# Optimization experiments

Measured on AMD Instinct MI355X. Metric: run time of the kernel, lower is better.

The kernel has to match this reference:

```python
import jax, jax.numpy as jnp
import numpy as np
from jax import lax


def _conv(x, w, b):
    # x: (B,C,H,W), w: (O,I,3,3) -> SAME padding, stride 1 (NCHW/OIHW)
    y = lax.conv_general_dilated(x, w, (1, 1), 'SAME',
                                 dimension_numbers=('NCHW', 'OIHW', 'NCHW'))
    return y + b[None, :, None, None]


def _maxpool2(x):
    return lax.reduce_window(x, -jnp.inf, lax.max, (1, 1, 2, 2), (1, 1, 2, 2), 'VALID')


def setup_inputs() -> dict:
    key = jax.random.key(0)
    ks = jax.random.split(key, 16)
    B, C, H, W = 4096, 3, 32, 32
    E, NC = 4, 10
    s = 0.05
    x = jax.random.normal(ks[0], (B, C, H, W), jnp.float32)
    return {
        'x': x,
        # gating network
        'gw_conv': jax.random.normal(ks[1], (16, C, 3, 3), jnp.float32) * s,
        'gb_conv': jnp.zeros((16,), jnp.float32),
        'gw_fc': jax.random.normal(ks[2], (E, 16), jnp.float32) * s,
        'gb_fc': jnp.zeros((E,), jnp.float32),
        # experts (stacked over leading expert dim E)
        'ew_conv1': jax.random.normal(ks[3], (E, 32, C, 3, 3), jnp.float32) * s,
        'eb_conv1': jnp.zeros((E, 32), jnp.float32),
        'ew_conv2': jax.random.normal(ks[4], (E, 64, 32, 3, 3), jnp.float32) * s,
        'eb_conv2': jnp.zeros((E, 64), jnp.float32),
        'ew_fc1': jax.random.normal(ks[5], (E, 128, 64 * 8 * 8), jnp.float32) * s,
        'eb_fc1': jnp.zeros((E, 128), jnp.float32),
        'ew_fc2': jax.random.normal(ks[6], (E, NC, 128), jnp.float32) * s,
        'eb_fc2': jnp.zeros((E, NC), jnp.float32),
    }


def reference(x, gw_conv, gb_conv, gw_fc, gb_fc,
              ew_conv1, eb_conv1, ew_conv2, eb_conv2,
              ew_fc1, eb_fc1, ew_fc2, eb_fc2):
    B = x.shape[0]
    E = gw_fc.shape[0]
    NC = ew_fc2.shape[1]
    TOP_K = 1

    # ---- Router: conv -> relu -> global avg pool -> linear -> softmax ----
    h = jax.nn.relu(_conv(x, gw_conv, gb_conv))          # (B,16,32,32)
    pooled = h.mean(axis=(2, 3))                          # (B,16)
    router_probs = jax.nn.softmax(pooled @ gw_fc.T + gb_fc, axis=1)  # (B,E)

    # ---- Top-k hard routing -> dense per-expert combine weights ----
    topk_probs, topk_idx = lax.top_k(router_probs, TOP_K)  # (B,k)
    weights = jnp.zeros((B, E), x.dtype).at[
        jnp.arange(B)[:, None], topk_idx].add(topk_probs)  # (B,E), zero off-topk

    # ---- Experts: run each expert densely, weight, accumulate ----
    # (expert_out * 0 == 0 exactly, so this matches torch's gather/scatter-add)
    final = jnp.zeros((B, NC), x.dtype)
    for i in range(E):  # small fixed expert count
        h1 = _maxpool2(jax.nn.relu(_conv(x, ew_conv1[i], eb_conv1[i])))   # (B,32,16,16)
        h2 = _maxpool2(jax.nn.relu(_conv(h1, ew_conv2[i], eb_conv2[i])))  # (B,64,8,8)
        f = h2.reshape(B, -1)                                             # (B,4096)
        f = jax.nn.relu(f @ ew_fc1[i].T + eb_fc1[i])                      # (B,128)
        out = f @ ew_fc2[i].T + eb_fc2[i]                                 # (B,NC)
        final = final + out * weights[:, i:i + 1]

    # ---- Load-balancing auxiliary loss (MSE vs uniform) ----
    mean_probs = router_probs.mean(axis=0)
    aux_loss = jnp.mean((mean_probs - 1.0 / E) ** 2)
    return final, router_probs, aux_loss
```

## Files before the change

kernel.cpp:

```cpp
#include <hip/hip_runtime.h>
#include <hip/hip_bf16.h>
#include <cstdint>
#include <cstddef>

#define B_N 4096
typedef short short8 __attribute__((ext_vector_type(8)));
typedef float f32x4 __attribute__((ext_vector_type(4)));
typedef float f32x2 __attribute__((ext_vector_type(2)));

static constexpr size_t H2B_OFF    = 0;
static constexpr size_t POOLED_OFF = 8388608;
static constexpr size_t EIDX_OFF   = POOLED_OFF + (size_t)B_N * 16;
static constexpr size_t EW_OFF     = EIDX_OFF + B_N;
static constexpr size_t ORDER_OFF  = EW_OFF + B_N;
static constexpr size_t CNT_OFF    = ORDER_OFF + (size_t)4 * B_N;
static constexpr size_t PSUM_OFF   = CNT_OFF + 4;
static constexpr size_t W2R_OFF    = PSUM_OFF + 4;
static constexpr size_t W1R_OFF    = W2R_OFF + 36864;
static constexpr size_t W1C_OFF    = W1R_OFF + 1048576;

__device__ __forceinline__ unsigned int f2bf(float f) {
  unsigned int u = __float_as_uint(f);
  return (u + 0x7fffu + ((u >> 16) & 1u)) >> 16;
}
__device__ __forceinline__ unsigned int pkbf(float lo, float hi) {
  float2 f; f.x = lo; f.y = hi;
  __hip_bfloat162 b = __float22bfloat162_rn(f);
  union { __hip_bfloat162 b; unsigned u; } c; c.b = b; return c.u;
}

__global__ __launch_bounds__(256) void k_front(
    const float* __restrict__ wfc1, unsigned short* __restrict__ w1r,
    const float* __restrict__ wc2, unsigned short* __restrict__ w2r,
    const float* __restrict__ wc1, unsigned short* __restrict__ w1c,
    int* __restrict__ counts) {
  const int rb = blockIdx.x, t = threadIdx.x;
  if (rb < 2048) {
    const int i = rb * 256 + t;
    const float4 v = ((const float4*)wfc1)[i];
    ushort4 u;
    u.x = (unsigned short)f2bf(v.x); u.y = (unsigned short)f2bf(v.y);
    u.z = (unsigned short)f2bf(v.z); u.w = (unsigned short)f2bf(v.w);
    *(ushort4*)(w1r + 4 * (size_t)i) = u;
  } else if (rb < 2336) {
    if (rb == 2048 && t < 8) counts[t] = 0;
    const int i = (rb - 2048) * 256 + t;
    if (i < 4 * 9 * 64 * 32) {
      const int ic = i & 31, j = i >> 5;
      const int oc = j & 63, j2 = j >> 6;
      const int s = j2 % 9, e = j2 / 9;
      w2r[i] = (unsigned short)f2bf(wc2[(((size_t)e * 64 + oc) * 32 + ic) * 9 + s]);
    }
  } else {
    const int i = (rb - 2336) * 256 + t;
    if (i < 4096) {
      const int j = i & 7, n16 = (i >> 3) & 15, q = (i >> 7) & 3, nt = (i >> 9) & 1, e = i >> 10;
      const int k = q * 8 + j;
      float v = 0.f;
      if (k < 27) {
        const int ky = k / 9, c = k % 9, kx = c / 3, ic = c % 3;
        v = wc1[((e * 32 + nt * 16 + n16) * 3 + ic) * 9 + ky * 3 + kx];
      }
      w1c[i] = (unsigned short)f2bf(v);
    }
  }
}

__device__ __forceinline__ short8 gather_a(const float* __restrict__ base,
                                           const int* goff, bool isq1, bool isq3) {
  const float a0 = base[goff[0]];
  float       a1 = base[goff[0] + 1];
  const float b0 = base[goff[1]], b1 = base[goff[1] + 1];
  const float c0 = base[goff[2]], c1 = base[goff[2] + 1];
  const float d0 = base[goff[3]], d1 = base[goff[3] + 1];
  a1 = isq1 ? base[102] : a1;
  union { unsigned u[4]; short8 s; } r;
  r.u[0] = pkbf(a0, a1);
  r.u[1] = pkbf(b0, isq3 ? 0.f : b1);
  r.u[2] = isq3 ? 0u : pkbf(c0, c1);
  r.u[3] = isq3 ? 0u : pkbf(d0, d1);
  return r.s;
}

__global__ __launch_bounds__(256, 3) void k_experts_conv(const float* __restrict__ x,
    const float* __restrict__ gw, const float* __restrict__ gb,
    const float* __restrict__ gwfc, const float* __restrict__ gbfc,
    const unsigned short* __restrict__ w1c, const float* __restrict__ b1g,
    const unsigned short* __restrict__ w2r, const float* __restrict__ b2g,
    unsigned short* __restrict__ h2b, float* __restrict__ probs_out,
    float* __restrict__ ewt, int* __restrict__ counts, int* __restrict__ order) {
  __shared__ __align__(16) float xpi[3572];
  __shared__ __align__(16) unsigned short h1s[18 * 18 * 36];
  __shared__ float red[16 * 33];
  __shared__ float pooled_s[16];
  __shared__ int es;
  const int b = blockIdx.x, t = threadIdx.x;
  {
    uint4 z4 = make_uint4(0, 0, 0, 0);
    uint4* z1 = (uint4*)h1s;
    for (int i = t; i < 1458; i += 256) z1[i] = z4;
    uint4* z2 = (uint4*)xpi;
    for (int i = t; i < 893; i += 256) z2[i] = z4;
  }
  __syncthreads();
  const float4* x4 = (const float4*)(x + (size_t)b * 3072);
  for (int i = t; i < 768; i += 256) {
    float4 v = x4[i];
    int flat = i * 4, ic = flat >> 10, rem = flat & 1023, row = rem >> 5, col = rem & 31;
    float* d = &xpi[(row + 1) * 102 + (col + 1) * 3 + ic];
    d[0] = v.x; d[3] = v.y; d[6] = v.z; d[9] = v.w;
  }
  __syncthreads();
  {
    const int ty = t >> 4, tx = t & 15;
    f32x2 wp[3][4][3];
#pragma unroll
    for (int ic = 0; ic < 3; ++ic)
#pragma unroll
    for (int rr = 0; rr < 4; ++rr) {
      const float* p = &xpi[(2 * ty + rr) * 102 + (2 * tx) * 3 + ic];
      const float r0 = p[0], r1 = p[3], r2 = p[6], r3 = p[9];
      wp[ic][rr][0] = (f32x2){r0, r1};
      wp[ic][rr][1] = (f32x2){r1, r2};
      wp[ic][rr][2] = (f32x2){r2, r3};
    }
    float sums[16];
#pragma unroll
    for (int oc = 0; oc < 16; ++oc) {
      const float bias = gb[oc];
      f32x2 A0 = {bias, bias};
      f32x2 A1 = {bias, bias};
#pragma unroll
      for (int ic = 0; ic < 3; ++ic)
#pragma unroll
      for (int ky = 0; ky < 3; ++ky)
#pragma unroll
      for (int kx = 0; kx < 3; ++kx) {
        const float wv2 = gw[oc * 27 + ic * 9 + ky * 3 + kx];
        const f32x2 ws = {wv2, wv2};
        A0 = __builtin_elementwise_fma(wp[ic][ky][kx], ws, A0);
        A1 = __builtin_elementwise_fma(wp[ic][ky + 1][kx], ws, A1);
      }
      sums[oc] = fmaxf(A0.x, 0.f) + fmaxf(A0.y, 0.f) + fmaxf(A1.x, 0.f) + fmaxf(A1.y, 0.f);
    }
    const int rl = t & 63, wid = t >> 6;
#pragma unroll
    for (int oc = 0; oc < 16; ++oc) {
      float s = sums[oc];
      s += __shfl_xor(s, 1);
      s += __shfl_xor(s, 2);
      s += __shfl_xor(s, 4);
      sums[oc] = s;
    }
    if ((rl & 7) == 0) {
      const int slot = wid * 8 + (rl >> 3);
#pragma unroll
      for (int oc = 0; oc < 16; ++oc) red[oc * 33 + slot] = sums[oc];
    }
    __syncthreads();
    if (t < 16) {
      float s = 0.f;
#pragma unroll
      for (int i = 0; i < 32; ++i) s += red[t * 33 + i];
      pooled_s[t] = s * (1.f / 1024.f);
    }
    __syncthreads();
    if (t == 0) {
      float l[4];
#pragma unroll
      for (int j = 0; j < 4; ++j) {
        float s = gbfc[j];
#pragma unroll
        for (int i = 0; i < 16; ++i) s += pooled_s[i] * gwfc[j * 16 + i];
        l[j] = s;
      }
      const float mx = fmaxf(fmaxf(l[0], l[1]), fmaxf(l[2], l[3]));
      float ex[4], ssum = 0.f;
#pragma unroll
      for (int j = 0; j < 4; ++j) { ex[j] = expf(l[j] - mx); ssum += ex[j]; }
      const float inv = 1.f / ssum;
      float p[4];
#pragma unroll
      for (int j = 0; j < 4; ++j) p[j] = ex[j] * inv;
      *(float4*)(probs_out + (size_t)b * 4) = make_float4(p[0], p[1], p[2], p[3]);
      int em = 0; float pm = p[0];
#pragma unroll
      for (int j = 1; j < 4; ++j) if (p[j] > pm) { pm = p[j]; em = j; }
      ewt[b] = pm;
      const int slot = atomicAdd(&counts[em], 1);
      order[em * B_N + slot] = b;
      es = em;
    }
    __syncthreads();
  }
  const int e = __builtin_amdgcn_readfirstlane(es);
  const int lane = t & 63, wv = t >> 6;
  const int n16 = lane & 15, q = lane >> 4;
  {
    const bool isq1 = (q == 1), isq3 = (q == 3);
    const short8 wb0 = *(const short8*)(w1c + (((e * 2 + 0) * 4 + q) * 16 + n16) * 8);
    const short8 wb1 = *(const short8*)(w1c + (((e * 2 + 1) * 4 + q) * 16 + n16) * 8);
    const float bias0 = b1g[e * 32 + n16];
    const float bias1 = b1g[e * 32 + 16 + n16];
    int goff[4];
#pragma unroll
    for (int t4 = 0; t4 < 4; ++t4) {
      const int p0 = q * 8 + 2 * t4;
      const int r = (p0 * 939) >> 13;
      goff[t4] = r * 102 + (p0 - 9 * r);
    }
    for (int pid = 0; pid < 8; ++pid) {
      const int pairid = wv * 8 + pid;
      const int yp = pairid >> 1, xh = pairid & 1;
      const float* baseA = &xpi[(2 * yp) * 102 + (xh * 16 + n16) * 3];
      const short8 afA = gather_a(baseA, goff, isq1, isq3);
      const short8 afB = gather_a(baseA + 102, goff, isq1, isq3);
      f32x4 aA0 = {bias0, bias0, bias0, bias0}, aA1 = {bias1, bias1, bias1, bias1};
      f32x4 aB0 = aA0, aB1 = aA1;
      aA0 = __builtin_amdgcn_mfma_f32_16x16x32_bf16(afA, wb0, aA0, 0, 0, 0);
      aA1 = __builtin_amdgcn_mfma_f32_16x16x32_bf16(afA, wb1, aA1, 0, 0, 0);
      aB0 = __builtin_amdgcn_mfma_f32_16x16x32_bf16(afB, wb0, aB0, 0, 0, 0);
      aB1 = __builtin_amdgcn_mfma_f32_16x16x32_bf16(afB, wb1, aB1, 0, 0, 0);
      const int px = xh * 8 + 2 * q;
      unsigned short* hw = &h1s[((yp + 1) * 18 + (px + 1)) * 36];
      const float p00 = fmaxf(fmaxf(fmaxf(aA0[0], aA0[1]), fmaxf(aB0[0], aB0[1])), 0.f);
      const float p01 = fmaxf(fmaxf(fmaxf(aA0[2], aA0[3]), fmaxf(aB0[2], aB0[3])), 0.f);
      const float p10 = fmaxf(fmaxf(fmaxf(aA1[0], aA1[1]), fmaxf(aB1[0], aB1[1])), 0.f);
      const float p11 = fmaxf(fmaxf(fmaxf(aA1[2], aA1[3]), fmaxf(aB1[2], aB1[3])), 0.f);
      hw[n16]           = (unsigned short)f2bf(p00);
      hw[16 + n16]      = (unsigned short)f2bf(p10);
      hw[36 + n16]      = (unsigned short)f2bf(p01);
      hw[36 + 16 + n16] = (unsigned short)f2bf(p11);
    }
  }
  __syncthreads();
  {
    const unsigned short* wbase = w2r + (size_t)e * 18432 + n16 * 32 + q * 8;
    float bz[4];
#pragma unroll
    for (int nt = 0; nt < 4; ++nt) bz[nt] = b2g[e * 64 + nt * 16 + n16];
    f32x4 acc[4][4];
#pragma unroll
    for (int mt4 = 0; mt4 < 4; ++mt4)
#pragma unroll
      for (int nt = 0; nt < 4; ++nt) {
        acc[mt4][nt][0] = bz[nt]; acc[mt4][nt][1] = bz[nt];
        acc[mt4][nt][2] = bz[nt]; acc[mt4][nt][3] = bz[nt];
      }
    short8 Bc[4];
#pragma unroll
    for (int nt = 0; nt < 4; ++nt) Bc[nt] = *(const short8*)(wbase + nt * 512);
#pragma unroll
    for (int s = 0; s < 9; ++s) {
      const int ky = s / 3, kx = s % 3;
      short8 Bn[4];
      if (s < 8) {
#pragma unroll
        for (int nt = 0; nt < 4; ++nt)
          Bn[nt] = *(const short8*)(wbase + (s + 1) * 2048 + nt * 512);
      }
#pragma unroll
      for (int mt4 = 0; mt4 < 4; ++mt4) {
        const int mt = wv * 4 + mt4;
        const short8 af = *(const short8*)&h1s[((mt + ky) * 18 + n16 + kx) * 36 + q * 8];
#pragma unroll
        for (int nt = 0; nt < 4; ++nt)
          acc[mt4][nt] = __builtin_amdgcn_mfma_f32_16x16x32_bf16(af, Bc[nt], acc[mt4][nt], 0, 0, 0);
      }
      if (s < 8) {
#pragma unroll
        for (int nt = 0; nt < 4; ++nt) Bc[nt] = Bn[nt];
      }
    }
    __syncthreads();
    float* h2s = (float*)h1s;
#pragma unroll
    for (int u2 = 0; u2 < 2; ++u2) {
      const int py = wv * 2 + u2;
#pragma unroll
      for (int nt = 0; nt < 4; ++nt) {
        const f32x4 a = acc[2 * u2][nt], c = acc[2 * u2 + 1][nt];
        float2 pv;
        pv.x = fmaxf(fmaxf(fmaxf(a[0], a[1]), fmaxf(c[0], c[1])), 0.f);
        pv.y = fmaxf(fmaxf(fmaxf(a[2], a[3]), fmaxf(c[2], c[3])), 0.f);
        *(float2*)&h2s[(nt * 16 + n16) * 68 + py * 8 + 2 * q] = pv;
      }
    }
  }
  __syncthreads();
  {
    const float* h2s = (const float*)h1s;
    unsigned short* dst = h2b + (size_t)b * 4096;
#pragma unroll
    for (int j = 0; j < 2; ++j) {
      const int f = 8 * (t + 256 * j);
      const float* src = &h2s[(f >> 6) * 68 + (f & 63)];
      float4 v0 = *(const float4*)src;
      float4 v1 = *(const float4*)(src + 4);
      unsigned int p0 = pkbf(v0.x, v0.y);
      unsigned int p1 = pkbf(v0.z, v0.w);
      unsigned int p2 = pkbf(v1.x, v1.y);
      unsigned int p3 = pkbf(v1.z, v1.w);
      *(uint4*)(dst + f) = make_uint4(p0, p1, p2, p3);
    }
  }
}

__global__ __launch_bounds__(512) void k_fc(const unsigned short* __restrict__ h2b,
    const unsigned short* __restrict__ w1r, const float* __restrict__ b1g,
    const float* __restrict__ w2g, const float* __restrict__ b2g,
    const int* __restrict__ counts, const int* __restrict__ order,
    const float* __restrict__ ew, float* __restrict__ outp) {
  const int bid = blockIdx.x;
  const int t = threadIdx.x;
  __shared__ float ax[4][4];
  if (bid == 0) {
    if (t < 256) {
      const float* pr = outp + 40960;
      float s0 = 0.f, s1 = 0.f, s2 = 0.f, s3 = 0.f;
      for (int i = t; i < 4096; i += 256) {
        const float4 v = *(const float4*)(pr + (size_t)i * 4);
        s0 += v.x; s1 += v.y; s2 += v.z; s3 += v.w;
      }
#pragma unroll
      for (int k = 1; k < 64; k <<= 1) {
        s0 += __shfl_xor(s0, k); s1 += __shfl_xor(s1, k);
        s2 += __shfl_xor(s2, k); s3 += __shfl_xor(s3, k);
      }
      if ((t & 63) == 0) {
        const int w = t >> 6;
        ax[w][0] = s0; ax[w][1] = s1; ax[w][2] = s2; ax[w][3] = s3;
      }
    }
    __syncthreads();
    if (t == 0) {
      float a = 0.f;
#pragma unroll
      for (int j = 0; j < 4; ++j) {
        const float mp = (ax[0][j] + ax[1][j] + ax[2][j] + ax[3][j]) * (1.f / 4096.f) - 0.25f;
        a += mp * mp;
      }
      outp[57344] = a * 0.25f;
    }
  }
  const int e = bid >> 8, tile = bid & 255;
  const int n = counts[e];
  const int base = tile * 16;
  if (base >= n) return;
  __shared__ int sb[16];
  __shared__ float wgt[16];
  __shared__ __align__(16) unsigned short As[16][280];
  __shared__ float f1s[16 * 132];
  if (t < 16) {
    const int idx = base + t;
    const int s = order[e * B_N + ((idx < n) ? idx : base)];
    sb[t] = s; wgt[t] = ew[s];
  }
  __syncthreads();
  const int lane = t & 63, wv = t >> 6;
  const int n16 = lane & 15, q = lane >> 4;
  const int oc = wv * 16 + n16;
  const unsigned short* wb = w1r + ((size_t)(e * 128 + oc)) * 4096 + q * 8;
  f32x4 acc = {0.f, 0.f, 0.f, 0.f};
  const int ldrow = t >> 5, ldseg = t & 31;
  const unsigned short* asrc = h2b + (size_t)sb[ldrow] * 4096;
  uint4 r0 = *(const uint4*)(asrc + ldseg * 8);
  for (int kc = 0; kc < 4096; kc += 256) {
    *(uint4*)&As[ldrow][ldseg * 8] = r0;
    __syncthreads();
    if (kc + 256 < 4096) {
      r0 = *(const uint4*)(asrc + (kc + 256) + ldseg * 8);
    }
#pragma unroll
    for (int ks = 0; ks < 8; ++ks) {
      const short8 af = *(const short8*)&As[n16][ks * 32 + q * 8];
      const short8 bf = *(const short8*)(wb + kc + ks * 32);
      acc = __builtin_amdgcn_mfma_f32_16x16x32_bf16(af, bf, acc, 0, 0, 0);
    }
    __syncthreads();
  }
  const float bb = b1g[e * 128 + oc];
#pragma unroll
  for (int r = 0; r < 4; ++r) {
    const int m = q * 4 + r;
    f1s[m * 132 + oc] = fmaxf(acc[r] + bb, 0.f);
  }
  __syncthreads();
  int m = n - base; if (m > 16) m = 16;
  if (t < 160) {
    const int r = t / 10, o = t - r * 10;
    if (r < m) {
      const float* w2 = w2g + (e * 10 + o) * 128;
      float s = b2g[e * 10 + o];
#pragma unroll 8
      for (int c = 0; c < 128; ++c) s += f1s[r * 132 + c] * w2[c];
      outp[(size_t)sb[r] * 10 + o] = s * wgt[r];
    }
  }
}

extern "C" void kernel_launch(void* const* d_in, const int* in_sizes, int n_in,
                              void* d_out, int out_size, void* d_ws, size_t ws_size,
                              hipStream_t stream) {
  const float* x        = (const float*)d_in[0];
  const float* gw_conv  = (const float*)d_in[1];
  const float* gb_conv  = (const float*)d_in[2];
  const float* gw_fc    = (const float*)d_in[3];
  const float* gb_fc    = (const float*)d_in[4];
  const float* ew_conv1 = (const float*)d_in[5];
  const float* eb_conv1 = (const float*)d_in[6];
  const float* ew_conv2 = (const float*)d_in[7];
  const float* eb_conv2 = (const float*)d_in[8];
  const float* ew_fc1   = (const float*)d_in[9];
  const float* eb_fc1   = (const float*)d_in[10];
  const float* ew_fc2   = (const float*)d_in[11];
  const float* eb_fc2   = (const float*)d_in[12];
  float* out = (float*)d_out;
  float* ws  = (float*)d_ws;

  unsigned short* h2b = (unsigned short*)(ws + H2B_OFF);
  float* ew     = ws + EW_OFF;
  int*   order  = (int*)(ws + ORDER_OFF);
  int*   counts = (int*)(ws + CNT_OFF);
  unsigned short* w2r = (unsigned short*)(ws + W2R_OFF);
  unsigned short* w1r = (unsigned short*)(ws + W1R_OFF);
  unsigned short* w1c = (unsigned short*)(ws + W1C_OFF);

  k_front<<<2352, 256, 0, stream>>>(ew_fc1, w1r, ew_conv2, w2r, ew_conv1, w1c, counts);
  k_experts_conv<<<4096, 256, 0, stream>>>(x, gw_conv, gb_conv, gw_fc, gb_fc,
                                           w1c, eb_conv1, w2r, eb_conv2, h2b,
                                           out + 40960, ew, counts, order);
  k_fc<<<1024, 512, 0, stream>>>(h2b, w1r, eb_fc1, ew_fc2, eb_fc2,
                                 counts, order, ew, out);
}
```

Measured before the change: 244.6 us.

## Move router conv and softmax into front kernel, pass expert index via workspace

The gating conv, pooling, softmax and top-1 selection move out of the expert conv kernel into the front weight-prep kernel, which gains 4096 extra blocks, one per sample. The front kernel writes an expert index to workspace, and the expert kernel reads it and does the counts/order atomics. This lightens the expert kernel's work and shared memory and removes its barriers, aiming to improve occupancy. The cost is a second full read of x and an extra global round-trip for the index.

After: 265.0 us. +8.4%, slower.

```diff
diff --git a/kernel.cpp b/kernel.cpp
--- a/kernel.cpp
+++ b/kernel.cpp
@@ -6,7 +6,6 @@
 #define B_N 4096
 typedef short short8 __attribute__((ext_vector_type(8)));
 typedef float f32x4 __attribute__((ext_vector_type(4)));
-typedef float f32x2 __attribute__((ext_vector_type(2)));
 
 static constexpr size_t H2B_OFF    = 0;
 static constexpr size_t POOLED_OFF = 8388608;
@@ -29,40 +28,134 @@
   union { __hip_bfloat162 b; unsigned u; } c; c.b = b; return c.u;
 }
 
-__global__ __launch_bounds__(256) void k_front(
+__global__ __launch_bounds__(256) void k_front(const float* __restrict__ x,
+    const float* __restrict__ gw, const float* __restrict__ gb,
+    const float* __restrict__ gwfc, const float* __restrict__ gbfc,
     const float* __restrict__ wfc1, unsigned short* __restrict__ w1r,
     const float* __restrict__ wc2, unsigned short* __restrict__ w2r,
     const float* __restrict__ wc1, unsigned short* __restrict__ w1c,
-    int* __restrict__ counts) {
-  const int rb = blockIdx.x, t = threadIdx.x;
-  if (rb < 2048) {
-    const int i = rb * 256 + t;
-    const float4 v = ((const float4*)wfc1)[i];
-    ushort4 u;
-    u.x = (unsigned short)f2bf(v.x); u.y = (unsigned short)f2bf(v.y);
-    u.z = (unsigned short)f2bf(v.z); u.w = (unsigned short)f2bf(v.w);
-    *(ushort4*)(w1r + 4 * (size_t)i) = u;
-  } else if (rb < 2336) {
-    if (rb == 2048 && t < 8) counts[t] = 0;
-    const int i = (rb - 2048) * 256 + t;
-    if (i < 4 * 9 * 64 * 32) {
-      const int ic = i & 31, j = i >> 5;
-      const int oc = j & 63, j2 = j >> 6;
-      const int s = j2 % 9, e = j2 / 9;
-      w2r[i] = (unsigned short)f2bf(wc2[(((size_t)e * 64 + oc) * 32 + ic) * 9 + s]);
-    }
-  } else {
-    const int i = (rb - 2336) * 256 + t;
-    if (i < 4096) {
-      const int j = i & 7, n16 = (i >> 3) & 15, q = (i >> 7) & 3, nt = (i >> 9) & 1, e = i >> 10;
-      const int k = q * 8 + j;
-      float v = 0.f;
-      if (k < 27) {
-        const int ky = k / 9, c = k % 9, kx = c / 3, ic = c % 3;
-        v = wc1[((e * 32 + nt * 16 + n16) * 3 + ic) * 9 + ky * 3 + kx];
-      }
-      w1c[i] = (unsigned short)f2bf(v);
-    }
+    int* __restrict__ counts, float* __restrict__ probs_out,
+    float* __restrict__ ewt, int* __restrict__ eidx) {
+  __shared__ __align__(16) float xpad[3 * 34 * 34];
+  __shared__ float red[16 * 33];
+  __shared__ float pooled_s[16];
+  const int bid = blockIdx.x, t = threadIdx.x;
+  if (bid >= 4096) {
+    const int rb = bid - 4096;
+    if (rb < 2048) {
+      const int i = rb * 256 + t;
+      const float4 v = ((const float4*)wfc1)[i];
+      ushort4 u;
+      u.x = (unsigned short)f2bf(v.x); u.y = (unsigned short)f2bf(v.y);
+      u.z = (unsigned short)f2bf(v.z); u.w = (unsigned short)f2bf(v.w);
+      *(ushort4*)(w1r + 4 * (size_t)i) = u;
+    } else if (rb < 2336) {
+      if (rb == 2048 && t < 8) counts[t] = 0;
+      const int i = (rb - 2048) * 256 + t;
+      if (i < 4 * 9 * 64 * 32) {
+        const int ic = i & 31, j = i >> 5;
+        const int oc = j & 63, j2 = j >> 6;
+        const int s = j2 % 9, e = j2 / 9;
+        w2r[i] = (unsigned short)f2bf(wc2[(((size_t)e * 64 + oc) * 32 + ic) * 9 + s]);
+      }
+    } else {
+      const int i = (rb - 2336) * 256 + t;
+      if (i < 4096) {
+        const int j = i & 7, n16 = (i >> 3) & 15, q = (i >> 7) & 3, nt = (i >> 9) & 1, e = i >> 10;
+        const int k = q * 8 + j;
+        float v = 0.f;
+        if (k < 27) {
+          const int ky = k / 9, c = k % 9, kx = c / 3, ic = c % 3;
+          v = wc1[((e * 32 + nt * 16 + n16) * 3 + ic) * 9 + ky * 3 + kx];
+        }
+        w1c[i] = (unsigned short)f2bf(v);
+      }
+    }
+    return;
+  }
+  const int b = bid;
+  for (int i = t; i < 867; i += 256) ((uint4*)xpad)[i] = make_uint4(0, 0, 0, 0);
+  __syncthreads();
+  const float4* x4 = (const float4*)(x + (size_t)b * 3072);
+  for (int i = t; i < 768; i += 256) {
+    float4 v = x4[i];
+    int flat = i * 4, ic = flat >> 10, rem = flat & 1023, row = rem >> 5, col = rem & 31;
+    float* d = &xpad[ic * 1156 + (row + 1) * 34 + (col + 1)];
+    d[0] = v.x; d[1] = v.y; d[2] = v.z; d[3] = v.w;
+  }
+  __syncthreads();
+  const int ty = t >> 4, tx = t & 15;
+  float win[3][4][4];
+#pragma unroll
+  for (int ic = 0; ic < 3; ++ic)
+#pragma unroll
+  for (int rr = 0; rr < 4; ++rr) {
+    const float2* p = (const float2*)&xpad[ic * 1156 + (2 * ty + rr) * 34 + 2 * tx];
+    float2 a = p[0], c = p[1];
+    win[ic][rr][0] = a.x; win[ic][rr][1] = a.y; win[ic][rr][2] = c.x; win[ic][rr][3] = c.y;
+  }
+  float sums[16];
+#pragma unroll
+  for (int oc = 0; oc < 16; ++oc) {
+    const float bias = gb[oc];
+    float a00 = bias, a01 = bias, a10 = bias, a11 = bias;
+#pragma unroll
+    for (int ic = 0; ic < 3; ++ic)
+#pragma unroll
+    for (int ky = 0; ky < 3; ++ky)
+#pragma unroll
+    for (int kx = 0; kx < 3; ++kx) {
+      const float wv = gw[oc * 27 + ic * 9 + ky * 3 + kx];
+      a00 += wv * win[ic][ky][kx];     a01 += wv * win[ic][ky][kx + 1];
+      a10 += wv * win[ic][ky + 1][kx]; a11 += wv * win[ic][ky + 1][kx + 1];
+    }
+    sums[oc] = fmaxf(a00, 0.f) + fmaxf(a01, 0.f) + fmaxf(a10, 0.f) + fmaxf(a11, 0.f);
+  }
+  const int lane = t & 63, wid = t >> 6;
+#pragma unroll
+  for (int oc = 0; oc < 16; ++oc) {
+    float s = sums[oc];
+    s += __shfl_xor(s, 1);
+    s += __shfl_xor(s, 2);
+    s += __shfl_xor(s, 4);
+    sums[oc] = s;
+  }
+  if ((lane & 7) == 0) {
+    const int slot = wid * 8 + (lane >> 3);
+#pragma unroll
+    for (int oc = 0; oc < 16; ++oc) red[oc * 33 + slot] = sums[oc];
+  }
+  __syncthreads();
+  if (t < 16) {
+    float s = 0.f;
+#pragma unroll
+    for (int i = 0; i < 32; ++i) s += red[t * 33 + i];
+    pooled_s[t] = s * (1.f / 1024.f);
+  }
+  __syncthreads();
+  if (t == 0) {
+    float l[4];
+#pragma unroll
+    for (int j = 0; j < 4; ++j) {
+      float s = gbfc[j];
+#pragma unroll
+      for (int i = 0; i < 16; ++i) s += pooled_s[i] * gwfc[j * 16 + i];
+      l[j] = s;
+    }
+    const float mx = fmaxf(fmaxf(l[0], l[1]), fmaxf(l[2], l[3]));
+    float ex[4], ssum = 0.f;
+#pragma unroll
+    for (int j = 0; j < 4; ++j) { ex[j] = expf(l[j] - mx); ssum += ex[j]; }
+    const float inv = 1.f / ssum;
+    float p[4];
+#pragma unroll
+    for (int j = 0; j < 4; ++j) p[j] = ex[j] * inv;
+    *(float4*)(probs_out + (size_t)b * 4) = make_float4(p[0], p[1], p[2], p[3]);
+    int em = 0; float pm = p[0];
+#pragma unroll
+    for (int j = 1; j < 4; ++j) if (p[j] > pm) { pm = p[j]; em = j; }
+    ewt[b] = pm;
+    eidx[b] = em;
   }
 }
 
@@ -83,18 +176,18 @@
 }
 
 __global__ __launch_bounds__(256, 3) void k_experts_conv(const float* __restrict__ x,
-    const float* __restrict__ gw, const float* __restrict__ gb,
-    const float* __restrict__ gwfc, const float* __restrict__ gbfc,
     const unsigned short* __restrict__ w1c, const float* __restrict__ b1g,
     const unsigned short* __restrict__ w2r, const float* __restrict__ b2g,
-    unsigned short* __restrict__ h2b, float* __restrict__ probs_out,
-    float* __restrict__ ewt, int* __restrict__ counts, int* __restrict__ order) {
+    const int* __restrict__ eidx, unsigned short* __restrict__ h2b,
+    int* __restrict__ counts, int* __restrict__ order) {
   __shared__ __align__(16) float xpi[3572];
   __shared__ __align__(16) unsigned short h1s[18 * 18 * 36];
-  __shared__ float red[16 * 33];
-  __shared__ float pooled_s[16];
-  __shared__ int es;
   const int b = blockIdx.x, t = threadIdx.x;
+  const int e = __builtin_amdgcn_readfirstlane(eidx[b]);
+  if (t == 0) {
+    const int slot = atomicAdd(&counts[e], 1);
+    order[e * B_N + slot] = b;
+  }
   {
     uint4 z4 = make_uint4(0, 0, 0, 0);
     uint4* z1 = (uint4*)h1s;
@@ -111,89 +204,6 @@
     d[0] = v.x; d[3] = v.y; d[6] = v.z; d[9] = v.w;
   }
   __syncthreads();
-  {
-    const int ty = t >> 4, tx = t & 15;
-    f32x2 wp[3][4][3];
-#pragma unroll
-    for (int ic = 0; ic < 3; ++ic)
-#pragma unroll
-    for (int rr = 0; rr < 4; ++rr) {
-      const float* p = &xpi[(2 * ty + rr) * 102 + (2 * tx) * 3 + ic];
-      const float r0 = p[0], r1 = p[3], r2 = p[6], r3 = p[9];
-      wp[ic][rr][0] = (f32x2){r0, r1};
-      wp[ic][rr][1] = (f32x2){r1, r2};
-      wp[ic][rr][2] = (f32x2){r2, r3};
-    }
-    float sums[16];
-#pragma unroll
-    for (int oc = 0; oc < 16; ++oc) {
-      const float bias = gb[oc];
-      f32x2 A0 = {bias, bias};
-      f32x2 A1 = {bias, bias};
-#pragma unroll
-      for (int ic = 0; ic < 3; ++ic)
-#pragma unroll
-      for (int ky = 0; ky < 3; ++ky)
-#pragma unroll
-      for (int kx = 0; kx < 3; ++kx) {
-        const float wv2 = gw[oc * 27 + ic * 9 + ky * 3 + kx];
-        const f32x2 ws = {wv2, wv2};
-        A0 = __builtin_elementwise_fma(wp[ic][ky][kx], ws, A0);
-        A1 = __builtin_elementwise_fma(wp[ic][ky + 1][kx], ws, A1);
-      }
-      sums[oc] = fmaxf(A0.x, 0.f) + fmaxf(A0.y, 0.f) + fmaxf(A1.x, 0.f) + fmaxf(A1.y, 0.f);
-    }
-    const int rl = t & 63, wid = t >> 6;
-#pragma unroll
-    for (int oc = 0; oc < 16; ++oc) {
-      float s = sums[oc];
-      s += __shfl_xor(s, 1);
-      s += __shfl_xor(s, 2);
-      s += __shfl_xor(s, 4);
-      sums[oc] = s;
-    }
-    if ((rl & 7) == 0) {
-      const int slot = wid * 8 + (rl >> 3);
-#pragma unroll
-      for (int oc = 0; oc < 16; ++oc) red[oc * 33 + slot] = sums[oc];
-    }
-    __syncthreads();
-    if (t < 16) {
-      float s = 0.f;
-#pragma unroll
-      for (int i = 0; i < 32; ++i) s += red[t * 33 + i];
-      pooled_s[t] = s * (1.f / 1024.f);
-    }
-    __syncthreads();
-    if (t == 0) {
-      float l[4];
-#pragma unroll
-      for (int j = 0; j < 4; ++j) {
-        float s = gbfc[j];
-#pragma unroll
-        for (int i = 0; i < 16; ++i) s += pooled_s[i] * gwfc[j * 16 + i];
-        l[j] = s;
-      }
-      const float mx = fmaxf(fmaxf(l[0], l[1]), fmaxf(l[2], l[3]));
-      float ex[4], ssum = 0.f;
-#pragma unroll
-      for (int j = 0; j < 4; ++j) { ex[j] = expf(l[j] - mx); ssum += ex[j]; }
-      const float inv = 1.f / ssum;
-      float p[4];
-#pragma unroll
-      for (int j = 0; j < 4; ++j) p[j] = ex[j] * inv;
-      *(float4*)(probs_out + (size_t)b * 4) = make_float4(p[0], p[1], p[2], p[3]);
-      int em = 0; float pm = p[0];
-#pragma unroll
-      for (int j = 1; j < 4; ++j) if (p[j] > pm) { pm = p[j]; em = j; }
-      ewt[b] = pm;
-      const int slot = atomicAdd(&counts[em], 1);
-      order[em * B_N + slot] = b;
-      es = em;
-    }
-    __syncthreads();
-  }
-  const int e = __builtin_amdgcn_readfirstlane(es);
   const int lane = t & 63, wv = t >> 6;
   const int n16 = lane & 15, q = lane >> 4;
   {
@@ -419,6 +429,7 @@
   float* ws  = (float*)d_ws;
 
   unsigned short* h2b = (unsigned short*)(ws + H2B_OFF);
+  int*   eidx   = (int*)(ws + EIDX_OFF);
   float* ew     = ws + EW_OFF;
   int*   order  = (int*)(ws + ORDER_OFF);
   int*   counts = (int*)(ws + CNT_OFF);
@@ -426,10 +437,11 @@
   unsigned short* w1r = (unsigned short*)(ws + W1R_OFF);
   unsigned short* w1c = (unsigned short*)(ws + W1C_OFF);
 
-  k_front<<<2352, 256, 0, stream>>>(ew_fc1, w1r, ew_conv2, w2r, ew_conv1, w1c, counts);
-  k_experts_conv<<<4096, 256, 0, stream>>>(x, gw_conv, gb_conv, gw_fc, gb_fc,
-                                           w1c, eb_conv1, w2r, eb_conv2, h2b,
-                                           out + 40960, ew, counts, order);
+  k_front<<<6448, 256, 0, stream>>>(x, gw_conv, gb_conv, gw_fc, gb_fc,
+                                    ew_fc1, w1r, ew_conv2, w2r, ew_conv1, w1c,
+                                    counts, out + 40960, ew, eidx);
+  k_experts_conv<<<4096, 256, 0, stream>>>(x, w1c, eb_conv1, w2r, eb_conv2,
+                                           eidx, h2b, counts, order);
   k_fc<<<1024, 512, 0, stream>>>(h2b, w1r, eb_fc1, ew_fc2, eb_fc2,
                                  counts, order, ew, out);
 }
```
